# Kernel tuning notes

Hardware: AMD Instinct MI355X
Metric: run time of the kernel (lower is better)

The kernel has to match this reference:

```python
import jax, jax.numpy as jnp
import numpy as np

N = 1024      # num_nodes
E = 4096      # edges (before self-loops)
HEADS = 8
B = 32
T = 64
HL = 512      # lstm_hidden_size (LSTMCell)
HR = 64       # hid_dim_lstmrr (rainfall LSTM)


def setup_inputs() -> dict:
    key = jax.random.key(0)
    ks = jax.random.split(key, 20)
    rn = lambda i, shape, s=0.05: (jax.random.normal(ks[i], shape, jnp.float32) * s)
    return dict(
        rainfall=rn(0, (B, T, 1), 1.0),
        inflow=rn(1, (B, T, 1), 1.0),
        edge_index=jax.random.randint(ks[2], (2, E), 0, N),
        lstm_Wih=rn(3, (4 * HR, 1)), lstm_Whh=rn(4, (4 * HR, HR)),
        lstm_bih=jnp.zeros(4 * HR), lstm_bhh=jnp.zeros(4 * HR),
        fc_W=rn(5, (N, HR)), fc_b=jnp.zeros(N),
        g1_W=rn(6, (3, HEADS * 3)), g1_as=rn(7, (HEADS, 3)), g1_ad=rn(8, (HEADS, 3)), g1_b=jnp.zeros(HEADS * 3),
        g2_W=rn(9, (24, HEADS * 2)), g2_as=rn(10, (HEADS, 2)), g2_ad=rn(11, (HEADS, 2)), g2_b=jnp.zeros(2),
        cell_Wih=rn(12, (4 * HL, 2 * N)), cell_Whh=rn(13, (4 * HL, HL)),
        cell_bih=jnp.zeros(4 * HL), cell_bhh=jnp.zeros(4 * HL),
        ln_g=jnp.ones(HL), ln_b=jnp.zeros(HL),
        lin_W=rn(14, (2 * N, HL)), lin_b=jnp.zeros(2 * N),
    )


def _gat(h_in, W, a_s, a_d, bias, src, dst, heads, oc, concat):
    # PyG GATConv: shared lin for src/dst, per-head attention, edge softmax by dst.
    n = h_in.shape[0]
    h = (h_in @ W).reshape(n, heads, oc)                       # [N, H, oc]
    logit = jax.nn.leaky_relu(jnp.sum(h * a_s, -1)[src] + jnp.sum(h * a_d, -1)[dst], 0.2)  # [Etot, H]
    m = jax.ops.segment_max(logit, dst, num_segments=n)
    e = jnp.exp(logit - m[dst])
    denom = jax.ops.segment_sum(e, dst, num_segments=n)
    alpha = e / (denom[dst] + 1e-16)                           # [Etot, H]
    out = jax.ops.segment_sum(h[src] * alpha[:, :, None], dst, num_segments=n)
    out = out.reshape(n, heads * oc) if concat else out.mean(1)
    return out + bias, alpha


def reference(rainfall, inflow, lstm_Wih, lstm_Whh, lstm_bih, lstm_bhh, fc_W, fc_b,
              g1_W, g1_as, g1_ad, g1_b, g2_W, g2_as, g2_ad, g2_b,
              cell_Wih, cell_Whh, cell_bih, cell_bhh, ln_g, ln_b, lin_W, lin_b, edge_index):
    Bb, Tt, _ = rainfall.shape
    loops = jnp.arange(N, dtype=edge_index.dtype)
    src = jnp.concatenate([edge_index[0], loops])              # PyG adds self-loops
    dst = jnp.concatenate([edge_index[1], loops])

    # rainfall LSTM (batch_first), gates ordered i,f,g,o as in torch
    def lstm_step(carry, xt):
        h, c = carry
        g = xt @ lstm_Wih.T + h @ lstm_Whh.T + lstm_bih + lstm_bhh
        i, f, gg, o = jnp.split(g, 4, -1)
        c = jax.nn.sigmoid(f) * c + jax.nn.sigmoid(i) * jnp.tanh(gg)
        h = jax.nn.sigmoid(o) * jnp.tanh(c)
        return (h, c), h
    z = jnp.zeros((Bb, HR), rainfall.dtype)
    _, hs = jax.lax.scan(lstm_step, (z, z), rainfall.transpose(1, 0, 2))   # [T, B, HR]
    runoff = jax.nn.leaky_relu(hs @ fc_W.T + fc_b, 0.01)                   # [T, B, N]
    runoff = runoff.at[:, :, 753].add(inflow.transpose(1, 0, 2)[:, :, 0])

    gat1 = jax.vmap(lambda x: _gat(x, g1_W, g1_as, g1_ad, g1_b, src, dst, HEADS, 3, True))
    gat2 = jax.vmap(lambda x: _gat(x, g2_W, g2_as, g2_ad, g2_b, src, dst, HEADS, 2, False))

    def step(carry, r_t):
        hn, cn, xn = carry
        lateral = r_t[:, :, None]                              # [B, N, 1]
        x = jnp.concatenate([xn, lateral], -1)                 # [B, N, 3]
        x1, att = gat1(x)
        x1 = jax.nn.leaky_relu(x1, 0.01)
        x2, _ = gat2(x1)
        x2 = jax.nn.leaky_relu(x2, 0.01)
        xf = x2.reshape(Bb, 2 * N)
        g = xf @ cell_Wih.T + hn @ cell_Whh.T + cell_bih + cell_bhh
        i, f, gg, o = jnp.split(g, 4, -1)
        cn = jax.nn.sigmoid(f) * cn + jax.nn.sigmoid(i) * jnp.tanh(gg)
        hn = jax.nn.sigmoid(o) * jnp.tanh(cn)
        mu = hn.mean(-1, keepdims=True)
        var = ((hn - mu) ** 2).mean(-1, keepdims=True)
        hn = (hn - mu) / jnp.sqrt(var + 1e-5) * ln_g + ln_b
        xn_flat = jax.nn.softplus(hn @ lin_W.T + lin_b)        # [B, 2N]
        return (hn, cn, xn_flat.reshape(Bb, N, 2)), (xn_flat, lateral, att)

    hn0 = jnp.zeros((Bb, HL), rainfall.dtype)
    cn0 = jnp.zeros((Bb, HL), rainfall.dtype)
    xn0 = jnp.zeros((Bb, N, 2), rainfall.dtype)
    _, (pred, lat, att) = jax.lax.scan(step, (hn0, cn0, xn0), runoff)
    prediction = pred.transpose(1, 0, 2)                       # [B, T, 2N]
    Lateral = lat.transpose(1, 0, 2, 3)                        # [B, T, N, 1]
    return prediction, Lateral, att                            # att: [T, B, E+N, HEADS]
```

## Files before the change

kernel.cpp:

```cpp
#include <hip/hip_runtime.h>
#include <hip/hip_bf16.h>

#define BB 32
#define TT 64
#define NNODE 1024
#define EE 4096
#define NEDGE 5120
#define NHEAD 8
#define HLL 512
#define HRR 64
#define TWO_N 2048
#define KCELL 2560

__device__ __forceinline__ float sigmoidf_(float x){ return 1.f/(1.f+expf(-x)); }
__device__ __forceinline__ float leaky(float x, float s){ return x>0.f? x : s*x; }

__global__ __launch_bounds__(1024) void k_csr_off(const int* __restrict__ ei, int* __restrict__ off){
  __shared__ int deg[NNODE];
  __shared__ int scn[NNODE];
  int tid = threadIdx.x;
  deg[tid] = 1;
  __syncthreads();
  for(int e=tid; e<EE; e+=1024) atomicAdd(&deg[ei[EE+e]], 1);
  __syncthreads();
  scn[tid] = deg[tid];
  __syncthreads();
  for(int ofs=1; ofs<1024; ofs<<=1){
    int add = (tid>=ofs)? scn[tid-ofs] : 0;
    __syncthreads();
    scn[tid] += add;
    __syncthreads();
  }
  off[tid+1] = scn[tid];
  if(tid==0) off[0] = 0;
}

__global__ __launch_bounds__(1024) void k_csr_fill(const int* __restrict__ ei,
    const int* __restrict__ off, int* __restrict__ adjp){
  __shared__ int dstb[EE];
  int tid = threadIdx.x;
  for(int e=tid; e<EE; e+=1024) dstb[e] = ei[EE+e];
  __syncthreads();
  int e = blockIdx.x*1024 + tid;
  int myd = dstb[e];
  int rank = 0;
  for(int ep=0; ep<e; ep++) rank += (dstb[ep]==myd) ? 1 : 0;
  adjp[off[myd]+rank] = (ei[e] << 13) | e;
  if(blockIdx.x==0) adjp[off[tid+1]-1] = (tid << 13) | (EE + tid);
}

__global__ __launch_bounds__(256) void k_lstm(
    const float* __restrict__ rain, const float* __restrict__ Wih,
    const float* __restrict__ Whh, const float* __restrict__ bih,
    const float* __restrict__ bhh, float* __restrict__ hs){
  int b = blockIdx.x;
  int j = threadIdx.x;
  __shared__ float h_lds[HRR];
  __shared__ float g_lds[4*HRR];
  float wh[HRR];
  #pragma unroll
  for(int k=0;k<HRR;k++) wh[k] = Whh[j*HRR+k];
  float wi = Wih[j];
  float bias = bih[j] + bhh[j];
  float c = 0.f;
  if(j < HRR) h_lds[j] = 0.f;
  __syncthreads();
  for(int t=0;t<TT;t++){
    float x = rain[b*TT+t];
    float g = fmaf(wi, x, bias);
    #pragma unroll
    for(int k=0;k<HRR;k++) g = fmaf(wh[k], h_lds[k], g);
    g_lds[j] = g;
    __syncthreads();
    if(j < HRR){
      c = sigmoidf_(g_lds[HRR+j])*c + sigmoidf_(g_lds[j])*tanhf(g_lds[2*HRR+j]);
      float h = sigmoidf_(g_lds[3*HRR+j])*tanhf(c);
      h_lds[j] = h;
      hs[(t*BB+b)*HRR + j] = h;
    }
    __syncthreads();
  }
}

__global__ __launch_bounds__(256) void k_runoff(
    const float* __restrict__ hs, const float* __restrict__ fcW,
    const float* __restrict__ fcb, const float* __restrict__ inflow,
    float* __restrict__ runoff, float* __restrict__ lat){
  int p = blockIdx.x;
  int q = p & 3; int tb = p >> 2; int t = tb >> 5; int b = tb & 31;
  int n = q*256 + threadIdx.x;
  __shared__ float hrow[HRR];
  if(threadIdx.x < HRR) hrow[threadIdx.x] = hs[(t*BB+b)*HRR + threadIdx.x];
  __syncthreads();
  const float* wrow = fcW + n*HRR;
  float a0=0,a1=0,a2=0,a3=0;
  #pragma unroll
  for(int k=0;k<HRR;k+=4){
    float4 w = *reinterpret_cast<const float4*>(wrow + k);
    a0 = fmaf(w.x, hrow[k+0], a0);
    a1 = fmaf(w.y, hrow[k+1], a1);
    a2 = fmaf(w.z, hrow[k+2], a2);
    a3 = fmaf(w.w, hrow[k+3], a3);
  }
  float acc = (a0+a1)+(a2+a3) + fcb[n];
  float r = leaky(acc, 0.01f);
  if(n == 753) r += inflow[b*TT + t];
  runoff[(t*BB+b)*NNODE + n] = r;
  lat[(size_t)(b*TT+t)*NNODE + n] = r;
}

__global__ __launch_bounds__(256) void k_prep0(const float* __restrict__ runoff,
    const float* __restrict__ g1W, const float* __restrict__ g1as, const float* __restrict__ g1ad,
    float* __restrict__ h1, float* __restrict__ s1, float* __restrict__ d1){
  int idx = blockIdx.x*256 + threadIdx.x;
  int b = idx >> 10; int n = idx & 1023;
  float x2 = runoff[b*NNODE + n];
  float hv[24];
  size_t base = (size_t)b*NNODE + n;
  #pragma unroll
  for(int o=0;o<24;o++){
    hv[o] = x2*g1W[48+o];
    h1[base*24+o] = hv[o];
  }
  #pragma unroll
  for(int hd=0; hd<NHEAD; hd++){
    float s=0.f, d=0.f;
    #pragma unroll
    for(int c=0;c<3;c++){
      float v = hv[hd*3+c];
      s = fmaf(v, g1as[hd*3+c], s);
      d = fmaf(v, g1ad[hd*3+c], d);
    }
    s1[base*8+hd] = s; d1[base*8+hd] = d;
  }
}

__global__ __launch_bounds__(256) void k_gat1f(
    const int* __restrict__ adjp, const int* __restrict__ off,
    const float* __restrict__ h1, const float* __restrict__ s1, const float* __restrict__ d1,
    const float* __restrict__ g1b, const float* __restrict__ g2W,
    const float* __restrict__ g2as, const float* __restrict__ g2ad,
    float* __restrict__ h2, float* __restrict__ s2, float* __restrict__ d2,
    float* __restrict__ att, int t){
  int tid = threadIdx.x;
  int g = tid >> 3; int hd = tid & 7;
  int p = blockIdx.x*32 + g;
  int b = p >> 10; int n = p & 1023;
  __shared__ float ss[NNODE*NHEAD];
  __shared__ float x1buf[32][25];
  size_t bbase = (size_t)b*NNODE;
  for(int i=tid; i<NNODE*NHEAD; i+=256) ss[i] = s1[bbase*8 + i];
  __syncthreads();
  int o0 = off[n], o1 = off[n+1];
  float dn = d1[(bbase+n)*8+hd];
  float m = -1e30f, den = 0.f;
  for(int idx=o0; idx<o1; idx++){
    int pk = adjp[idx]; int s = pk >> 13;
    float lg = leaky(ss[s*8+hd] + dn, 0.2f);
    if(lg > m){ den *= expf(m - lg); m = lg; }
    den += expf(lg - m);
  }
  float inv = 1.f/(den + 1e-16f);
  float o_0=0.f, o_1=0.f, o_2=0.f;
  for(int idx=o0; idx<o1; idx++){
    int pk = adjp[idx]; int s = pk >> 13; int eid = pk & 8191;
    float lg = leaky(ss[s*8+hd] + dn, 0.2f);
    float al = expf(lg - m)*inv;
    att[((size_t)(t*BB+b)*NEDGE + eid)*NHEAD + hd] = al;
    const float* hr = h1 + (bbase+s)*24 + hd*3;
    o_0 = fmaf(hr[0], al, o_0);
    o_1 = fmaf(hr[1], al, o_1);
    o_2 = fmaf(hr[2], al, o_2);
  }
  x1buf[g][hd*3+0] = leaky(o_0 + g1b[hd*3+0], 0.01f);
  x1buf[g][hd*3+1] = leaky(o_1 + g1b[hd*3+1], 0.01f);
  x1buf[g][hd*3+2] = leaky(o_2 + g1b[hd*3+2], 0.01f);
  __syncthreads();
  float h2v0=0.f, h2v1=0.f;
  int oA = hd*2, oB = hd*2+1;
  #pragma unroll
  for(int k=0;k<24;k++){
    float xv = x1buf[g][k];
    h2v0 = fmaf(xv, g2W[k*16+oA], h2v0);
    h2v1 = fmaf(xv, g2W[k*16+oB], h2v1);
  }
  h2[(bbase+n)*16+oA] = h2v0;
  h2[(bbase+n)*16+oB] = h2v1;
  s2[(bbase+n)*8+hd] = h2v0*g2as[oA] + h2v1*g2as[oB];
  d2[(bbase+n)*8+hd] = h2v0*g2ad[oA] + h2v1*g2ad[oB];
}

__global__ __launch_bounds__(256) void k_gat2f(
    const int* __restrict__ adjp, const int* __restrict__ off,
    const float* __restrict__ h2, const float* __restrict__ s2, const float* __restrict__ d2,
    const float* __restrict__ g2b, float* __restrict__ xf){
  int tid = threadIdx.x;
  int g = tid >> 3; int hd = tid & 7;
  int p = blockIdx.x*32 + g;
  int b = p >> 10; int n = p & 1023;
  __shared__ float ss[NNODE*NHEAD];
  __shared__ float outbuf[32][17];
  size_t bbase = (size_t)b*NNODE;
  for(int i=tid; i<NNODE*NHEAD; i+=256) ss[i] = s2[bbase*8 + i];
  __syncthreads();
  int o0 = off[n], o1 = off[n+1];
  float dn = d2[(bbase+n)*8+hd];
  float m = -1e30f, den = 0.f;
  for(int idx=o0; idx<o1; idx++){
    int pk = adjp[idx]; int s = pk >> 13;
    float lg = leaky(ss[s*8+hd] + dn, 0.2f);
    if(lg > m){ den *= expf(m - lg); m = lg; }
    den += expf(lg - m);
  }
  float inv = 1.f/(den + 1e-16f);
  float o_0=0.f, o_1=0.f;
  for(int idx=o0; idx<o1; idx++){
    int pk = adjp[idx]; int s = pk >> 13;
    float lg = leaky(ss[s*8+hd] + dn, 0.2f);
    float al = expf(lg - m)*inv;
    const float* hr = h2 + (bbase+s)*16 + hd*2;
    o_0 = fmaf(hr[0], al, o_0);
    o_1 = fmaf(hr[1], al, o_1);
  }
  outbuf[g][hd*2+0] = o_0;
  outbuf[g][hd*2+1] = o_1;
  __syncthreads();
  if(hd < 2){
    float acc = 0.f;
    #pragma unroll
    for(int k=0;k<8;k++) acc += outbuf[g][k*2+hd];
    float v = leaky(acc*0.125f + g2b[hd], 0.01f);
    xf[b*TWO_N + n*2 + hd] = v;
  }
}

__global__ __launch_bounds__(256) void k_cellgate(const float* __restrict__ xf,
    const float* __restrict__ hn, const float* __restrict__ Wih, const float* __restrict__ Whh,
    const float* __restrict__ bih, const float* __restrict__ bhh,
    float* __restrict__ cn, float* __restrict__ hraw, float* __restrict__ stats){
  __shared__ float xl[256*33];
  const int q = blockIdx.x;
  const int tid = threadIdx.x;
  const int jl = tid >> 5;
  const int b  = tid & 31;
  const int j  = (jl>>1)*512 + q*2 + (jl&1);
  float a0=0,a1=0,a2=0,a3=0;
  for(int k0=0; k0<KCELL; k0+=256){
    if(k0 < TWO_N){
      for(int i=0;i<32;i++) xl[tid*33+i] = xf[i*TWO_N + k0 + tid];
    } else {
      for(int i=0;i<32;i++) xl[tid*33+i] = hn[i*HLL + (k0-TWO_N) + tid];
    }
    __syncthreads();
    const float* wrow = (k0 < TWO_N) ? (Wih + (size_t)j*TWO_N + k0)
                                     : (Whh + (size_t)j*HLL + (k0-TWO_N));
    #pragma unroll 4
    for(int kk=0; kk<256; kk+=8){
      float4 w0 = *reinterpret_cast<const float4*>(wrow + kk);
      float4 w1 = *reinterpret_cast<const float4*>(wrow + kk + 4);
      const float* xp = &xl[kk*33 + b];
      a0 = fmaf(w0.x, xp[0],   a0);
      a1 = fmaf(w0.y, xp[33],  a1);
      a2 = fmaf(w0.z, xp[66],  a2);
      a3 = fmaf(w0.w, xp[99],  a3);
      a0 = fmaf(w1.x, xp[132], a0);
      a1 = fmaf(w1.y, xp[165], a1);
      a2 = fmaf(w1.z, xp[198], a2);
      a3 = fmaf(w1.w, xp[231], a3);
    }
    __syncthreads();
  }
  float gv = (a0+a1)+(a2+a3) + bih[j] + bhh[j];
  xl[jl*32 + b] = gv;
  __syncthreads();
  float hval = 0.f;
  if(jl < 2){
    int u = q*2 + jl;
    float gi = xl[(0+jl)*32 + b];
    float gf = xl[(2+jl)*32 + b];
    float gg = xl[(4+jl)*32 + b];
    float go = xl[(6+jl)*32 + b];
    float c = sigmoidf_(gf)*cn[b*HLL+u] + sigmoidf_(gi)*tanhf(gg);
    cn[b*HLL+u] = c;
    hval = sigmoidf_(go)*tanhf(c);
    hraw[b*HLL+u] = hval;
  }
  __syncthreads();
  if(jl < 2){
    xl[256 + jl*32 + b] = hval;
    xl[384 + jl*32 + b] = hval*hval;
  }
  __syncthreads();
  if(jl == 0){
    stats[(q*32 + b)*2 + 0] = xl[256 + b] + xl[288 + b];
    stats[(q*32 + b)*2 + 1] = xl[384 + b] + xl[416 + b];
  }
}

__global__ __launch_bounds__(256) void k_linln(const float* __restrict__ hraw,
    const float* __restrict__ stats, const float* __restrict__ lng, const float* __restrict__ lnb,
    float* __restrict__ hn,
    const float* __restrict__ W, const float* __restrict__ bias,
    const float* __restrict__ runoff, float* __restrict__ pred,
    float* __restrict__ h1, float* __restrict__ s1, float* __restrict__ d1,
    const float* __restrict__ g1W, const float* __restrict__ g1as, const float* __restrict__ g1ad,
    int t){
  __shared__ float hl[256*33];
  __shared__ float red1[256], red2[256];
  __shared__ float musd[32], rstds[32];
  const int q = blockIdx.x;
  const int tid = threadIdx.x;
  {
    int b8 = tid >> 3, l8 = tid & 7;
    float s = 0.f, s2 = 0.f;
    for(int qq = l8*32; qq < l8*32+32; qq++){
      s  += stats[(qq*32 + b8)*2 + 0];
      s2 += stats[(qq*32 + b8)*2 + 1];
    }
    red1[tid] = s; red2[tid] = s2;
    __syncthreads();
    if(l8 < 4){ red1[tid] += red1[tid+4]; red2[tid] += red2[tid+4]; }
    __syncthreads();
    if(l8 < 2){ red1[tid] += red1[tid+2]; red2[tid] += red2[tid+2]; }
    __syncthreads();
    if(l8 == 0){
      float S = red1[tid] + red1[tid+1];
      float S2 = red2[tid] + red2[tid+1];
      float mu = S * (1.f/HLL);
      float var = S2 * (1.f/HLL) - mu*mu;
      musd[b8] = mu;
      rstds[b8] = rsqrtf(var + 1e-5f);
    }
    __syncthreads();
  }
  if(tid < 64){
    int e = q*64 + tid; int b = e >> 9; int u = e & 511;
    hn[e] = (hraw[e] - musd[b])*rstds[b]*lng[u] + lnb[u];
  }
  int jl = tid >> 5; int b = tid & 31;
  int j = q*8 + jl;
  float a0=0.f,a1=0.f,a2=0.f,a3=0.f;
  for(int k0=0; k0<HLL; k0+=256){
    float lg_ = lng[k0+tid], lb_ = lnb[k0+tid];
    __syncthreads();
    for(int i=0;i<32;i++)
      hl[tid*33+i] = (hraw[i*HLL + k0 + tid] - musd[i])*rstds[i]*lg_ + lb_;
    __syncthreads();
    const float* wrow = W + (size_t)j*HLL + k0;
    #pragma unroll 4
    for(int kk=0; kk<256; kk+=8){
      float4 w0 = *reinterpret_cast<const float4*>(wrow + kk);
      float4 w1 = *reinterpret_cast<const float4*>(wrow + kk + 4);
      const float* xp = &hl[kk*33 + b];
      a0 = fmaf(w0.x, xp[0],   a0);
      a1 = fmaf(w0.y, xp[33],  a1);
      a2 = fmaf(w0.z, xp[66],  a2);
      a3 = fmaf(w0.w, xp[99],  a3);
      a0 = fmaf(w1.x, xp[132], a0);
      a1 = fmaf(w1.y, xp[165], a1);
      a2 = fmaf(w1.z, xp[198], a2);
      a3 = fmaf(w1.w, xp[231], a3);
    }
  }
  float val = (a0+a1)+(a2+a3) + bias[j];
  float sp = fmaxf(val, 0.f) + log1pf(expf(-fabsf(val)));
  pred[((size_t)b*TT + t)*TWO_N + j] = sp;
  if(t+1 < TT){
    float partner = __shfl_xor(sp, 32);
    if((jl & 1) == 0){
      int n = j >> 1;
      float x2 = runoff[(size_t)(t+1)*BB*NNODE + b*NNODE + n];
      float hv2[24];
      size_t base = (size_t)b*NNODE + n;
      #pragma unroll
      for(int o=0;o<24;o++){
        hv2[o] = sp*g1W[o] + partner*g1W[24+o] + x2*g1W[48+o];
        h1[base*24+o] = hv2[o];
      }
      #pragma unroll
      for(int hd=0; hd<NHEAD; hd++){
        float s=0.f, d=0.f;
        #pragma unroll
        for(int c2=0;c2<3;c2++){
          float v2 = hv2[hd*3+c2];
          s = fmaf(v2, g1as[hd*3+c2], s);
          d = fmaf(v2, g1ad[hd*3+c2], d);
        }
        s1[base*8+hd] = s; d1[base*8+hd] = d;
      }
    }
  }
}

__global__ __launch_bounds__(512) void k_init(float* __restrict__ hn, float* __restrict__ cn){
  int idx = blockIdx.x*512 + threadIdx.x;
  if(idx < BB*HLL) hn[idx] = 0.f;
  else cn[idx - BB*HLL] = 0.f;
}

extern "C" void kernel_launch(void* const* d_in, const int* in_sizes, int n_in,
                              void* d_out, int out_size, void* d_ws, size_t ws_size,
                              hipStream_t stream){
  const float* rainfall  = (const float*)d_in[0];
  const float* inflow    = (const float*)d_in[1];
  const int*   edge_index= (const int*)  d_in[2];
  const float* lstm_Wih  = (const float*)d_in[3];
  const float* lstm_Whh  = (const float*)d_in[4];
  const float* lstm_bih  = (const float*)d_in[5];
  const float* lstm_bhh  = (const float*)d_in[6];
  const float* fc_W      = (const float*)d_in[7];
  const float* fc_b      = (const float*)d_in[8];
  const float* g1_W      = (const float*)d_in[9];
  const float* g1_as     = (const float*)d_in[10];
  const float* g1_ad     = (const float*)d_in[11];
  const float* g1_b      = (const float*)d_in[12];
  const float* g2_W      = (const float*)d_in[13];
  const float* g2_as     = (const float*)d_in[14];
  const float* g2_ad     = (const float*)d_in[15];
  const float* g2_b      = (const float*)d_in[16];
  const float* cell_Wih  = (const float*)d_in[17];
  const float* cell_Whh  = (const float*)d_in[18];
  const float* cell_bih  = (const float*)d_in[19];
  const float* cell_bhh  = (const float*)d_in[20];
  const float* ln_g      = (const float*)d_in[21];
  const float* ln_b      = (const float*)d_in[22];
  const float* lin_W     = (const float*)d_in[23];
  const float* lin_b     = (const float*)d_in[24];

  float* out  = (float*)d_out;
  float* pred = out;
  float* lat  = out + (size_t)4194304;
  float* att  = out + (size_t)6291456;

  float* ws = (float*)d_ws;
  float* hs     = ws;
  float* runoff = hs + 131072;
  float* h1     = runoff + 2097152;
  float* s1     = h1 + 786432;
  float* d1     = s1 + 262144;
  float* h2     = d1 + 262144;
  float* s2     = h2 + 524288;
  float* d2     = s2 + 262144;
  float* xfb    = d2 + 262144;
  float* hraw   = xfb + 65536;
  float* stats  = hraw + 16384;
  float* hn     = stats + 16384;
  float* cn     = hn + 16384;
  int*   off    = (int*)(cn + 16384);
  int*   adjp   = off + 1032;
  if(ws_size < 18898976ull) return;

  k_init<<<64, 512, 0, stream>>>(hn, cn);
  k_csr_off<<<1, 1024, 0, stream>>>(edge_index, off);
  k_csr_fill<<<4, 1024, 0, stream>>>(edge_index, off, adjp);
  k_lstm<<<BB, 256, 0, stream>>>(rainfall, lstm_Wih, lstm_Whh, lstm_bih, lstm_bhh, hs);
  k_runoff<<<TT*BB*4, 256, 0, stream>>>(hs, fc_W, fc_b, inflow, runoff, lat);
  k_prep0<<<128, 256, 0, stream>>>(runoff, g1_W, g1_as, g1_ad, h1, s1, d1);

  for(int t=0; t<TT; t++){
    k_gat1f<<<1024, 256, 0, stream>>>(adjp, off, h1, s1, d1,
        g1_b, g2_W, g2_as, g2_ad, h2, s2, d2, att, t);
    k_gat2f<<<1024, 256, 0, stream>>>(adjp, off, h2, s2, d2, g2_b, xfb);
    k_cellgate<<<256, 256, 0, stream>>>(xfb, hn, cell_Wih, cell_Whh,
        cell_bih, cell_bhh, cn, hraw, stats);
    k_linln<<<256, 256, 0, stream>>>(hraw, stats, ln_g, ln_b, hn,
        lin_W, lin_b, runoff, pred, h1, s1, d1, g1_W, g1_as, g1_ad, t);
  }
}
```

Before: 6.363 ms.

## Split cell-gate K reduction across two blocks with atomic last-block epilogue

The LSTM cell gate GEMV is split along K into two halves, which doubles the grid from 256 to 512 blocks so more CUs stay busy. Each half writes partial gate sums to global scratch, and an atomic counter picks the second finisher per column group to combine them and run the LSTM nonlinearity and layer-norm stats. The stats layout is transposed to match. This adds global round trips, threadfences and atomics in exchange for more parallelism on a small-grid kernel.

```diff
diff --git a/kernel.cpp b/kernel.cpp
--- a/kernel.cpp
+++ b/kernel.cpp
@@ -237,15 +237,19 @@
 __global__ __launch_bounds__(256) void k_cellgate(const float* __restrict__ xf,
     const float* __restrict__ hn, const float* __restrict__ Wih, const float* __restrict__ Whh,
     const float* __restrict__ bih, const float* __restrict__ bhh,
-    float* __restrict__ cn, float* __restrict__ hraw, float* __restrict__ stats){
+    float* __restrict__ gp0, float* __restrict__ gp1,
+    float* __restrict__ cn, float* __restrict__ hraw, float* __restrict__ stats,
+    int* __restrict__ cnt){
   __shared__ float xl[256*33];
-  const int q = blockIdx.x;
-  const int tid = threadIdx.x;
-  const int jl = tid >> 5;
-  const int b  = tid & 31;
-  const int j  = (jl>>1)*512 + q*2 + (jl&1);
+  __shared__ int winner;
+  int bid = blockIdx.x;
+  int half = bid >> 8; int q = bid & 255;
+  int tid = threadIdx.x;
+  int jl = tid >> 5; int b = tid & 31;
+  int j = (jl>>1)*512 + q*2 + (jl&1);
   float a0=0,a1=0,a2=0,a3=0;
-  for(int k0=0; k0<KCELL; k0+=256){
+  int kbeg = half*1280, kend = kbeg + 1280;
+  for(int k0=kbeg; k0<kend; k0+=256){
     if(k0 < TWO_N){
       for(int i=0;i<32;i++) xl[tid*33+i] = xf[i*TWO_N + k0 + tid];
     } else {
@@ -270,30 +274,34 @@
     }
     __syncthreads();
   }
-  float gv = (a0+a1)+(a2+a3) + bih[j] + bhh[j];
-  xl[jl*32 + b] = gv;
-  __syncthreads();
-  float hval = 0.f;
-  if(jl < 2){
-    int u = q*2 + jl;
-    float gi = xl[(0+jl)*32 + b];
-    float gf = xl[(2+jl)*32 + b];
-    float gg = xl[(4+jl)*32 + b];
-    float go = xl[(6+jl)*32 + b];
-    float c = sigmoidf_(gf)*cn[b*HLL+u] + sigmoidf_(gi)*tanhf(gg);
-    cn[b*HLL+u] = c;
-    hval = sigmoidf_(go)*tanhf(c);
-    hraw[b*HLL+u] = hval;
-  }
-  __syncthreads();
-  if(jl < 2){
-    xl[256 + jl*32 + b] = hval;
-    xl[384 + jl*32 + b] = hval*hval;
-  }
-  __syncthreads();
-  if(jl == 0){
-    stats[(q*32 + b)*2 + 0] = xl[256 + b] + xl[288 + b];
-    stats[(q*32 + b)*2 + 1] = xl[384 + b] + xl[416 + b];
+  float* dst = half ? gp1 : gp0;
+  dst[b*TWO_N + j] = (a0+a1)+(a2+a3);
+  __threadfence();
+  if(tid==0) winner = atomicAdd(&cnt[q], 1);
+  __syncthreads();
+  if(winner == 1){
+    __threadfence();
+    float hval = 0.f;
+    int r = tid >> 5;
+    if(tid < 64){
+      int u = q*2 + r;
+      float gi = gp0[b*TWO_N + u]          + gp1[b*TWO_N + u]          + bih[u]        + bhh[u];
+      float gf = gp0[b*TWO_N + HLL + u]    + gp1[b*TWO_N + HLL + u]    + bih[HLL+u]    + bhh[HLL+u];
+      float gg = gp0[b*TWO_N + 2*HLL + u]  + gp1[b*TWO_N + 2*HLL + u]  + bih[2*HLL+u]  + bhh[2*HLL+u];
+      float go = gp0[b*TWO_N + 3*HLL + u]  + gp1[b*TWO_N + 3*HLL + u]  + bih[3*HLL+u]  + bhh[3*HLL+u];
+      float c = sigmoidf_(gf)*cn[b*HLL+u] + sigmoidf_(gi)*tanhf(gg);
+      cn[b*HLL+u] = c;
+      hval = sigmoidf_(go)*tanhf(c);
+      hraw[b*HLL+u] = hval;
+    }
+    __syncthreads();
+    if(tid < 64){ xl[tid] = hval; xl[64+tid] = hval*hval; }
+    __syncthreads();
+    if(tid < 32){
+      stats[tid*(2*256) + q*2 + 0] = xl[tid] + xl[32+tid];
+      stats[tid*(2*256) + q*2 + 1] = xl[64+tid] + xl[96+tid];
+    }
+    if(tid==0) atomicSub(&cnt[q], 2);
   }
 }
 
@@ -314,8 +322,8 @@
     int b8 = tid >> 3, l8 = tid & 7;
     float s = 0.f, s2 = 0.f;
     for(int qq = l8*32; qq < l8*32+32; qq++){
-      s  += stats[(qq*32 + b8)*2 + 0];
-      s2 += stats[(qq*32 + b8)*2 + 1];
+      s  += stats[b8*512 + qq*2 + 0];
+      s2 += stats[b8*512 + qq*2 + 1];
     }
     red1[tid] = s; red2[tid] = s2;
     __syncthreads();
@@ -442,14 +450,18 @@
   float* s2     = h2 + 524288;
   float* d2     = s2 + 262144;
   float* xfb    = d2 + 262144;
-  float* hraw   = xfb + 65536;
+  float* gp0    = xfb + 65536;
+  float* gp1    = gp0 + 65536;
+  float* hraw   = gp1 + 65536;
   float* stats  = hraw + 16384;
   float* hn     = stats + 16384;
   float* cn     = hn + 16384;
   int*   off    = (int*)(cn + 16384);
   int*   adjp   = off + 1032;
-  if(ws_size < 18898976ull) return;
-
+  int*   cnt    = adjp + 5120;
+  if(ws_size < 19424288ull) return;
+
+  hipMemsetAsync(cnt, 0, 256*sizeof(int), stream);
   k_init<<<64, 512, 0, stream>>>(hn, cn);
   k_csr_off<<<1, 1024, 0, stream>>>(edge_index, off);
   k_csr_fill<<<4, 1024, 0, stream>>>(edge_index, off, adjp);
@@ -461,8 +473,8 @@
     k_gat1f<<<1024, 256, 0, stream>>>(adjp, off, h1, s1, d1,
         g1_b, g2_W, g2_as, g2_ad, h2, s2, d2, att, t);
     k_gat2f<<<1024, 256, 0, stream>>>(adjp, off, h2, s2, d2, g2_b, xfb);
-    k_cellgate<<<256, 256, 0, stream>>>(xfb, hn, cell_Wih, cell_Whh,
-        cell_bih, cell_bhh, cn, hraw, stats);
+    k_cellgate<<<512, 256, 0, stream>>>(xfb, hn, cell_Wih, cell_Whh,
+        cell_bih, cell_bhh, gp0, gp1, cn, hraw, stats, cnt);
     k_linln<<<256, 256, 0, stream>>>(hraw, stats, ln_g, ln_b, hn,
         lin_W, lin_b, runoff, pred, h1, s1, d1, g1_W, g1_as, g1_ad, t);
   }
```

After: 9.433 ms. 48.2% more time.
